# Optimization experiments

Measured on AMD Instinct MI355X. Metric: run time of the kernel, lower is better.

Reference implementation:

```python
import jax, jax.numpy as jnp
import numpy as np

K0, K1, STRIDE, PADDING = 3, 3, 1, 2


def setup_inputs() -> dict:
    key = jax.random.key(0)
    k1, k2, k3 = jax.random.split(key, 3)
    x = jax.random.normal(k1, (4, 16, 64, 64), dtype=jnp.float32)
    # weights: (out_channels, accl_sz) where accl_sz = in_channels*k0*k1 = 16*9 = 144
    weights = jax.random.normal(k2, (64, 144), dtype=jnp.float32) * 0.1
    bias = jax.random.normal(k3, (64, 1, 1), dtype=jnp.float32) * 0.05
    return {"x": x, "weights": weights, "bias": bias}


def _unfold_patches(x):
    """Replicate-pad then extract (B,1,Hout,Wout,accl) patches, accl ordered (C,k0,k1)."""
    pad_l = PADDING // 2
    pad_r = PADDING - pad_l
    x_pad = jnp.pad(x, ((0, 0), (0, 0), (pad_l, pad_r), (pad_l, pad_r)), mode="edge")
    B, C, Hp, Wp = x_pad.shape
    Hout = (Hp - K0) // STRIDE + 1
    Wout = (Wp - K1) // STRIDE + 1
    rows = []
    for i in range(K0):  # fixed small kernel loop
        cols = []
        for j in range(K1):
            cols.append(x_pad[:, :, i:i + STRIDE * Hout:STRIDE, j:j + STRIDE * Wout:STRIDE])
        rows.append(jnp.stack(cols, axis=-1))  # (B,C,Hout,Wout,k1)
    patches = jnp.stack(rows, axis=-2)  # (B,C,Hout,Wout,k0,k1)
    patches = jnp.transpose(patches, (0, 2, 3, 1, 4, 5))  # (B,Hout,Wout,C,k0,k1)
    return patches.reshape(B, 1, Hout, Wout, C * K0 * K1)


def reference(x, weights, bias):
    patches = _unfold_patches(x)                 # (B,1,Hout,Wout,accl)
    w = weights[:, None, None, :]                # (Cout,1,1,accl)
    # p = inf: L-infinity distance between weight vector and each patch
    dist = jnp.max(jnp.abs(w - patches), axis=-1)  # (B,Cout,Hout,Wout)
    return dist + bias
```

## Files before the change

### kernel.cpp

```cpp
#include <hip/hip_runtime.h>


#define BB 4
#define CC 16
#define HH 64
#define WW 64
#define FF 64
#define FCHUNK 4

#define DPP_LEFT(v)  __int_as_float(__builtin_amdgcn_update_dpp(            \
        __float_as_int(v), __float_as_int(v), 0x138, 0xf, 0xf, false))
#define DPP_RIGHT(v) __int_as_float(__builtin_amdgcn_update_dpp(            \
        __float_as_int(v), __float_as_int(v), 0x130, 0xf, 0xf, false))

__global__ __launch_bounds__(256) void dist_conv2d_kernel(
    const float* __restrict__ x,
    const float* __restrict__ wgt,
    const float* __restrict__ bias,
    float* __restrict__ out) {
    int w  = threadIdx.x & 63;
    int h  = ((blockIdx.x & 15) << 2) | (threadIdx.x >> 6);
    int b  = (blockIdx.x >> 4) & 3;
    int fc = blockIdx.x >> 6;
    int f0 = fc * FCHUNK;

    int r0 = h - 1; if (r0 < 0) r0 = 0;
    int r2 = h + 1; if (r2 > HH - 1) r2 = HH - 1;
    int row0 = r0 * WW + w, row1 = h * WW + w, row2 = r2 * WW + w;

    float dist[FCHUNK];
#pragma unroll
    for (int i = 0; i < FCHUNK; ++i) dist[i] = 0.0f;

    const float* xb    = x + b * (CC * HH * WW);
    const float* wbase = wgt + f0 * (CC * 9);

#pragma unroll 4
    for (int c = 0; c < CC; ++c) {
        const float* xc = xb + c * (HH * WW);
        float v0 = xc[row0], v1 = xc[row1], v2 = xc[row2];
        float p[9];
        p[0] = DPP_LEFT(v0);  p[1] = v0;  p[2] = DPP_RIGHT(v0);
        p[3] = DPP_LEFT(v1);  p[4] = v1;  p[5] = DPP_RIGHT(v1);
        p[6] = DPP_LEFT(v2);  p[7] = v2;  p[8] = DPP_RIGHT(v2);
#pragma unroll
        for (int fi = 0; fi < FCHUNK; ++fi) {
            const float* wrow = wbase + fi * (CC * 9) + c * 9;
#pragma unroll
            for (int k = 0; k < 9; ++k) {
                float d = p[k] - wrow[k];
                dist[fi] = fmaxf(dist[fi], fabsf(d));
            }
        }
    }

    float* ob = out + ((b * FF + f0) * HH + h) * WW + w;
#pragma unroll
    for (int fi = 0; fi < FCHUNK; ++fi) {
        ob[fi * (HH * WW)] = dist[fi] + bias[f0 + fi];
    }
}

extern "C" void kernel_launch(void* const* d_in, const int* in_sizes, int n_in,
                              void* d_out, int out_size, void* d_ws, size_t ws_size,
                              hipStream_t stream) {
    const float* x    = (const float*)d_in[0];
    const float* wgt  = (const float*)d_in[1];
    const float* bias = (const float*)d_in[2];
    float* out = (float*)d_out;

    const int total = (FF / FCHUNK) * BB * HH * WW;
    dist_conv2d_kernel<<<total / 256, 256, 0, stream>>>(x, wgt, bias, out);
}
```

Baseline: 14.10 us.

## Compute two output rows per thread with packed f32 subtraction

Each thread now produces two adjacent output rows for two filters instead of one row for four. The subtraction of the broadcast weight from the patch values is done with inline-asm v_pk_add_f32 on row pairs, and the four loaded input rows are shared between both output rows. The aim is to cut the per-output VALU subtract count and reuse the vertical halo loads. In exchange it needs twice as many DPP shifts per channel, the max/abs work stays scalar, and the inline asm with an SGPR 64-bit operand may constrain scheduling or force extra moves.

```diff
diff --git a/kernel.cpp b/kernel.cpp
--- a/kernel.cpp
+++ b/kernel.cpp
@@ -6,58 +6,92 @@
 #define HH 64
 #define WW 64
 #define FF 64
-#define FCHUNK 4
+#define FCHUNK 2
+
+typedef float f32x2 __attribute__((ext_vector_type(2)));
 
 #define DPP_LEFT(v)  __int_as_float(__builtin_amdgcn_update_dpp(            \
         __float_as_int(v), __float_as_int(v), 0x138, 0xf, 0xf, false))
 #define DPP_RIGHT(v) __int_as_float(__builtin_amdgcn_update_dpp(            \
         __float_as_int(v), __float_as_int(v), 0x130, 0xf, 0xf, false))
 
+#define PKSUB(D, P, WV) do {                                                \
+        float _wf = (WV);                                                   \
+        unsigned int _wu = __float_as_uint(_wf);                            \
+        unsigned long long _w2 =                                            \
+            ((unsigned long long)_wu << 32) | (unsigned long long)_wu;      \
+        asm("v_pk_add_f32 %0, %1, %2 neg_lo:[0,1] neg_hi:[0,1]"             \
+            : "=v"(D) : "v"(P), "s"(_w2));                                  \
+    } while (0)
+
 __global__ __launch_bounds__(256) void dist_conv2d_kernel(
     const float* __restrict__ x,
     const float* __restrict__ wgt,
     const float* __restrict__ bias,
     float* __restrict__ out) {
-    int w  = threadIdx.x & 63;
-    int h  = ((blockIdx.x & 15) << 2) | (threadIdx.x >> 6);
-    int b  = (blockIdx.x >> 4) & 3;
-    int fc = blockIdx.x >> 6;
-    int f0 = fc * FCHUNK;
+    int w     = threadIdx.x & 63;
+    int hp_lo = threadIdx.x >> 6;
+    int hp_hi = blockIdx.x & 7;
+    int b     = (blockIdx.x >> 3) & 3;
+    int fc    = blockIdx.x >> 5;
+    int f0    = fc * FCHUNK;
 
-    int r0 = h - 1; if (r0 < 0) r0 = 0;
-    int r2 = h + 1; if (r2 > HH - 1) r2 = HH - 1;
-    int row0 = r0 * WW + w, row1 = h * WW + w, row2 = r2 * WW + w;
+    int hp = hp_hi * 4 + hp_lo;
+    int h0 = hp * 2;
+    int h1 = h0 + 1;
 
-    float dist[FCHUNK];
-#pragma unroll
-    for (int i = 0; i < FCHUNK; ++i) dist[i] = 0.0f;
+    int rt = (h0 == 0) ? 0 : h0 - 1;
+    int rb = (h1 == HH - 1) ? HH - 1 : h1 + 1;
+    int o_t = rt * WW + w, o_a = h0 * WW + w, o_b = h1 * WW + w, o_c = rb * WW + w;
 
     const float* xb    = x + b * (CC * HH * WW);
     const float* wbase = wgt + f0 * (CC * 9);
 
+    f32x2 acc[FCHUNK];
+#pragma unroll
+    for (int i = 0; i < FCHUNK; ++i) acc[i] = (f32x2)(0.0f, 0.0f);
+
 #pragma unroll 4
     for (int c = 0; c < CC; ++c) {
         const float* xc = xb + c * (HH * WW);
-        float v0 = xc[row0], v1 = xc[row1], v2 = xc[row2];
-        float p[9];
-        p[0] = DPP_LEFT(v0);  p[1] = v0;  p[2] = DPP_RIGHT(v0);
-        p[3] = DPP_LEFT(v1);  p[4] = v1;  p[5] = DPP_RIGHT(v1);
-        p[6] = DPP_LEFT(v2);  p[7] = v2;  p[8] = DPP_RIGHT(v2);
+        float va = xc[o_t], vb = xc[o_a], vc_ = xc[o_b], vd = xc[o_c];
+        f32x2 cp0, cp1, cp2, lp0, lp1, lp2, rp0, rp1, rp2;
+        cp0.x = va;  cp0.y = vb;
+        cp1.x = vb;  cp1.y = vc_;
+        cp2.x = vc_; cp2.y = vd;
+        lp0.x = DPP_LEFT(cp0.x);  lp0.y = DPP_LEFT(cp0.y);
+        lp1.x = DPP_LEFT(cp1.x);  lp1.y = DPP_LEFT(cp1.y);
+        lp2.x = DPP_LEFT(cp2.x);  lp2.y = DPP_LEFT(cp2.y);
+        rp0.x = DPP_RIGHT(cp0.x); rp0.y = DPP_RIGHT(cp0.y);
+        rp1.x = DPP_RIGHT(cp1.x); rp1.y = DPP_RIGHT(cp1.y);
+        rp2.x = DPP_RIGHT(cp2.x); rp2.y = DPP_RIGHT(cp2.y);
+
 #pragma unroll
         for (int fi = 0; fi < FCHUNK; ++fi) {
-            const float* wrow = wbase + fi * (CC * 9) + c * 9;
-#pragma unroll
-            for (int k = 0; k < 9; ++k) {
-                float d = p[k] - wrow[k];
-                dist[fi] = fmaxf(dist[fi], fabsf(d));
-            }
+            const float* wr = wbase + fi * (CC * 9) + c * 9;
+            f32x2 d0, d1, d2, d3, d4, d5, d6, d7, d8;
+            PKSUB(d0, lp0, wr[0]); PKSUB(d1, cp0, wr[1]); PKSUB(d2, rp0, wr[2]);
+            PKSUB(d3, lp1, wr[3]); PKSUB(d4, cp1, wr[4]); PKSUB(d5, rp1, wr[5]);
+            PKSUB(d6, lp2, wr[6]); PKSUB(d7, cp2, wr[7]); PKSUB(d8, rp2, wr[8]);
+            acc[fi].x = fmaxf(fmaxf(acc[fi].x, fabsf(d0.x)), fabsf(d1.x));
+            acc[fi].y = fmaxf(fmaxf(acc[fi].y, fabsf(d0.y)), fabsf(d1.y));
+            acc[fi].x = fmaxf(fmaxf(acc[fi].x, fabsf(d2.x)), fabsf(d3.x));
+            acc[fi].y = fmaxf(fmaxf(acc[fi].y, fabsf(d2.y)), fabsf(d3.y));
+            acc[fi].x = fmaxf(fmaxf(acc[fi].x, fabsf(d4.x)), fabsf(d5.x));
+            acc[fi].y = fmaxf(fmaxf(acc[fi].y, fabsf(d4.y)), fabsf(d5.y));
+            acc[fi].x = fmaxf(fmaxf(acc[fi].x, fabsf(d6.x)), fabsf(d7.x));
+            acc[fi].y = fmaxf(fmaxf(acc[fi].y, fabsf(d6.y)), fabsf(d7.y));
+            acc[fi].x = fmaxf(acc[fi].x, fabsf(d8.x));
+            acc[fi].y = fmaxf(acc[fi].y, fabsf(d8.y));
         }
     }
 
-    float* ob = out + ((b * FF + f0) * HH + h) * WW + w;
 #pragma unroll
     for (int fi = 0; fi < FCHUNK; ++fi) {
-        ob[fi * (HH * WW)] = dist[fi] + bias[f0 + fi];
+        float bv = bias[f0 + fi];
+        float* ob = out + ((b * FF + f0 + fi) * HH) * WW + w;
+        ob[h0 * WW] = acc[fi].x + bv;
+        ob[h1 * WW] = acc[fi].y + bv;
     }
 }
 
@@ -69,6 +103,5 @@
     const float* bias = (const float*)d_in[2];
     float* out = (float*)d_out;
 
-    const int total = (FF / FCHUNK) * BB * HH * WW;
-    dist_conv2d_kernel<<<total / 256, 256, 0, stream>>>(x, wgt, bias, out);
+    dist_conv2d_kernel<<<1024, 256, 0, stream>>>(x, wgt, bias, out);
 }
```

After: 14.75 us. +4.6%, slower.
